# Performance work log

Hardware: AMD Instinct MI355X
Metric: run time of the kernel (lower is better)

Reference implementation:

```python
import jax, jax.numpy as jnp
from jax import lax
import numpy as np

T_STEPS, C_IN, H_IN, W_IN = 15, 6, 256, 256
C_OUT, KSIZE = 64, 5
THRESH = 15.0   # conv_t[0]
KWTA = 5        # ks[0]
INH_R = 3       # inh_radiuses[0]


def setup_inputs() -> dict:
    key = jax.random.key(0)
    k1, k2 = jax.random.split(key)
    # cumulative binary spike-wave: once a unit spikes it stays on (SpykeTorch convention)
    bern = jax.random.uniform(k1, (T_STEPS, C_IN, H_IN, W_IN)) < 0.05
    spikes = (jnp.cumsum(bern.astype(jnp.int32), axis=0) > 0).astype(jnp.float32)
    # SpykeTorch Convolution init: N(0.8, 0.05)
    w1 = 0.8 + 0.05 * jax.random.normal(k2, (C_OUT, C_IN, KSIZE, KSIZE), dtype=jnp.float32)
    return {"input": spikes, "w1": w1, "current_layer_id": 1}


def pointwise_inhibition(thr_pot):
    # thr_pot: (T, C, H, W). Keep, at each spatial position, only the feature
    # with the earliest spike (ties broken by max potential); zero the rest.
    T = thr_pot.shape[0]
    C = thr_pot.shape[1]
    max_vals = jnp.max(thr_pot, axis=1, keepdims=True)            # (T,1,H,W)
    max_idx = jnp.argmax(thr_pot, axis=1, keepdims=True)          # (T,1,H,W)
    clamp_pot = jnp.sign(max_vals)                                # (T,1,H,W) in {0,1}
    earliest = jnp.clip((T - clamp_pot.sum(axis=0, keepdims=True)).astype(jnp.int32), 0, T - 1)  # (1,1,H,W)
    winners = jnp.take_along_axis(max_idx, earliest, axis=0)      # (1,1,H,W)
    onehot = (jnp.arange(C)[None, :, None, None] == winners[:, 0])  # (1,C,H,W)
    coef = onehot.astype(thr_pot.dtype) * clamp_pot[-1:]          # zero where no spike at last step
    return thr_pot * coef


def get_k_winners(pot, spk, kwta, inh_radius):
    # pot, spk: (T, C, H, W). Returns (kwta, 3) int winners (c, h, w); -1 rows = no winner.
    T, C, H, W = pot.shape
    earliest = jnp.clip((T - spk.sum(axis=0, keepdims=True)).astype(jnp.int32), 0, T - 1)
    values = jnp.take_along_axis(pot, earliest, axis=0)           # (1,C,H,W)
    trunc = spk * values
    v = trunc.max() * T
    trunc = trunc + spk * v
    total = trunc.sum(axis=0)                                     # (C,H,W)
    rows = jnp.arange(H)
    cols = jnp.arange(W)

    def step(total, _):
        idx = jnp.argmax(total)
        val = total.reshape(-1)[idx]
        c = idx // (H * W)
        rem = idx % (H * W)
        h = rem // W
        w = rem % W
        winner = jnp.where(val != 0,
                           jnp.stack([c, h, w]),
                           jnp.full((3,), -1, dtype=idx.dtype))
        total = total.at[c].set(0.0)
        box = (((rows >= h - inh_radius) & (rows <= h + inh_radius))[:, None]
               & ((cols >= w - inh_radius) & (cols <= w + inh_radius))[None, :])
        total = jnp.where(box[None, :, :], 0.0, total)            # columnar spatial inhibition
        return total, winner

    _, winners = lax.scan(step, total, None, length=kwta)
    return winners


def reference(input, w1, current_layer_id):
    # training path, current_layer_id == 1
    x = jnp.pad(input.astype(jnp.float32), ((0, 0), (0, 0), (2, 2), (2, 2)))  # sf.pad (2,2,2,2)
    pot = lax.conv_general_dilated(x, w1, (1, 1), 'VALID',
                                   dimension_numbers=('NCHW', 'OIHW', 'NCHW'))  # (T,64,256,256)
    pot = jnp.where(pot < THRESH, 0.0, pot)   # sf.fire -> thresholded potentials
    pot = pointwise_inhibition(pot)
    spk = jnp.sign(pot)
    winners = get_k_winners(pot, spk, KWTA, INH_R)
    return spk, pot, winners
```

## Files before the change

### kernel.cpp

```cpp
#include <hip/hip_runtime.h>
#include <stdint.h>

static constexpr int T_STEPS = 15;
static constexpr int C_IN = 6;
static constexpr int C_OUT = 64;
static constexpr int H = 256;
static constexpr int W = 256;
static constexpr int NPOS = H * W;
static constexpr int NTAP = 150;
#define DTHRESH 15.0

typedef float vfloat4 __attribute__((ext_vector_type(4)));

static constexpr size_t WS_FT     = 0;
static constexpr size_t WS_SERIES = 393216;
static constexpr size_t WS_WINC   = WS_SERIES + (size_t)NPOS*16*4;
static constexpr size_t WS_NMAP   = WS_WINC + (size_t)NPOS;
static constexpr size_t WS_VAL    = WS_NMAP + (size_t)NPOS;
static constexpr size_t WS_NEED   = WS_VAL + (size_t)NPOS*8;

__global__ __launch_bounds__(256) void ft_kernel(const float* __restrict__ x,
                                                 uint8_t* __restrict__ ft) {
    int i = blockIdx.x * 256 + threadIdx.x;
    if (i >= C_IN * NPOS) return;
    int f = 15;
    #pragma unroll
    for (int t = T_STEPS - 1; t >= 0; --t) {
        if (x[(size_t)t * (C_IN * NPOS) + i] > 0.0f) f = t;
    }
    ft[i] = (uint8_t)f;
}

__global__ __launch_bounds__(256, 4) void conv_kernel(
        const float* __restrict__ w1, const uint8_t* __restrict__ ftg,
        float* __restrict__ series_ws, int8_t* __restrict__ winc_ws,
        uint8_t* __restrict__ nmap_ws, double* __restrict__ val_ws)
{
    __shared__ float w_lds[NTAP * 64];
    __shared__ uint8_t ft_lds[6 * 5 * 20];
    __shared__ alignas(16) unsigned cnt_lds[4][16];
    __shared__ alignas(16) unsigned short sorted_lds[4][200];

    int tid = threadIdx.x;
    int bid = blockIdx.x;
    int h  = bid >> 4;
    int w0 = (bid & 15) << 4;

    for (int i = tid; i < C_OUT * NTAP; i += 256) {
        int o = i / NTAP;
        int tap = i - o * NTAP;
        w_lds[tap * 64 + o] = w1[i];
    }
    for (int i = tid; i < 600; i += 256) {
        int c = i / 100;
        int r = i - c * 100;
        int kh = r / 20;
        int j  = r - kh * 20;
        int gh = h - 2 + kh;
        int gw = w0 - 2 + j;
        uint8_t v = 15;
        if (gh >= 0 && gh < H && gw >= 0 && gw < W) v = ftg[c * NPOS + gh * W + gw];
        ft_lds[(c * 5 + kh) * 20 + j] = v;
    }
    __syncthreads();

    int lane = tid & 63;
    int wvi  = tid >> 6;
    unsigned* cnt = cnt_lds[wvi];
    unsigned short* srt = sorted_lds[wvi];

    for (int iter = 0; iter < 4; ++iter) {
        int xl = iter * 4 + wvi;
        int p  = h * W + w0 + xl;

        if (lane < 16) cnt[lane] = 0;

        int tap0 = lane, tap1 = lane + 64, tap2 = lane + 128;
        auto ftv = [&](int tap) -> unsigned {
            int c = tap / 25;
            int r = tap - c * 25;
            int kh = r / 5;
            int kw = r - kh * 5;
            return ft_lds[(c * 5 + kh) * 20 + xl + kw];
        };
        unsigned f0 = ftv(tap0);
        unsigned f1 = ftv(tap1);
        unsigned f2 = (tap2 < NTAP) ? ftv(tap2) : 15u;
        unsigned r0 = 0, r1 = 0, r2 = 0;
        if (f0 < 15u) r0 = atomicAdd(&cnt[f0], 1u);
        if (f1 < 15u) r1 = atomicAdd(&cnt[f1], 1u);
        if (f2 < 15u) r2 = atomicAdd(&cnt[f2], 1u);

        uint4 c4[4];
        #pragma unroll
        for (int i = 0; i < 4; ++i) c4[i] = ((const uint4*)cnt)[i];
        unsigned cv_t[16];
        #pragma unroll
        for (int i = 0; i < 4; ++i) {
            cv_t[4*i+0] = c4[i].x; cv_t[4*i+1] = c4[i].y;
            cv_t[4*i+2] = c4[i].z; cv_t[4*i+3] = c4[i].w;
        }
        int kt[15];
        #pragma unroll
        for (int t = 0; t < 15; ++t) kt[t] = (int)__builtin_amdgcn_readfirstlane(cv_t[t]);

        unsigned st0 = 0, st1 = 0, st2 = 0;
        #pragma unroll
        for (int t = 0; t < 15; ++t) {
            unsigned a = (cv_t[t] + 3u) & ~3u;
            if ((unsigned)t < f0) st0 += a;
            if ((unsigned)t < f1) st1 += a;
            if ((unsigned)t < f2) st2 += a;
        }
        if (f0 < 15u) srt[st0 + r0] = (unsigned short)(tap0 << 6);
        if (f1 < 15u) srt[st1 + r1] = (unsigned short)(tap1 << 6);
        if (f2 < 15u) srt[st2 + r2] = (unsigned short)(tap2 << 6);

        double run = 0.0, cvv = 0.0;
        int tc = 127;
        float ser[15];
        int A = 0;
        #pragma unroll
        for (int t = 0; t < 15; ++t) {
            int k = kt[t];
            for (int q = 0; q < k; q += 4) {
                uint2 pr = *(const uint2*)(srt + A + q);
                unsigned e0 = pr.x & 0xFFFFu, e1 = pr.x >> 16;
                unsigned e2 = pr.y & 0xFFFFu, e3 = pr.y >> 16;
                e0 = min(e0, 9536u); e1 = min(e1, 9536u);
                e2 = min(e2, 9536u); e3 = min(e3, 9536u);
                float wa = w_lds[e0 + lane];
                float wb = w_lds[e1 + lane];
                float wcf = w_lds[e2 + lane];
                float wd = w_lds[e3 + lane];
                double p0 = (double)wa;
                double p1 = (q + 1 < k) ? (double)wb : 0.0;
                double p2 = (q + 2 < k) ? (double)wcf : 0.0;
                double p3 = (q + 3 < k) ? (double)wd : 0.0;
                run += ((p0 + p1) + (p2 + p3));
            }
            A += (k + 3) & ~3;
            ser[t] = (float)run;
            bool cross_now = (tc == 127) && (run >= DTHRESH);
            if (cross_now) { tc = t; cvv = run; }
        }

        int e = tc;
        #pragma unroll
        for (int off = 32; off >= 1; off >>= 1) e = min(e, __shfl_xor(e, off));
        int wc = -1;
        double val = 0.0;
        if (e < 15) {
            double vl = (tc == e) ? cvv : 0.0;
            double m = vl;
            #pragma unroll
            for (int off = 32; off >= 1; off >>= 1) m = fmax(m, __shfl_xor(m, off));
            unsigned long long mk = __ballot(vl == m);
            wc = __ffsll(mk) - 1;
            val = m;

            float ov = 0.0f;
            #pragma unroll
            for (int t = 0; t < 15; ++t) {
                float sv = __shfl(ser[t], wc);
                if (lane == t) ov = sv;
            }
            if (lane < e) ov = 0.0f;
            if (lane < 15) series_ws[p * 16 + lane] = ov;
        }
        if (lane == 0) {
            winc_ws[p] = (int8_t)wc;
            nmap_ws[p] = (uint8_t)(wc >= 0 ? (15 - e) : 0);
            if (wc >= 0) val_ws[p] = val;
        }
    }
}

__global__ __launch_bounds__(1024) void kwin_kernel(
        const int8_t* __restrict__ winc, const uint8_t* __restrict__ nmap,
        const double* __restrict__ val, float* __restrict__ outw)
{
    __shared__ int8_t  winc_l[NPOS];
    __shared__ uint8_t nmap_l[NPOS];
    __shared__ double rv_lds[16];
    __shared__ unsigned ri_lds[16];
    __shared__ double v_lds;
    __shared__ int win_c[5], win_h[5], win_w[5];
    int tid = threadIdx.x, lane = tid & 63, wvi = tid >> 6;

    {
        const int4* ws4 = (const int4*)winc;
        int4* wd4 = (int4*)winc_l;
        const int4* ns4 = (const int4*)nmap;
        int4* nd4 = (int4*)nmap_l;
        #pragma unroll
        for (int i = 0; i < NPOS / 16 / 1024; ++i) {
            wd4[tid + (i << 10)] = ws4[tid + (i << 10)];
            nd4[tid + (i << 10)] = ns4[tid + (i << 10)];
        }
    }
    __syncthreads();

    double mv = 0.0;
    for (int k = 0; k < 64; ++k) {
        int p = (k << 10) + tid;
        if (winc_l[p] >= 0) mv = fmax(mv, val[p]);
    }
    #pragma unroll
    for (int off = 32; off >= 1; off >>= 1) mv = fmax(mv, __shfl_xor(mv, off));
    if (lane == 0) rv_lds[wvi] = mv;
    __syncthreads();
    if (tid == 0) {
        double m = rv_lds[0];
        for (int i = 1; i < 16; ++i) m = fmax(m, rv_lds[i]);
        v_lds = 15.0 * m;
    }
    __syncthreads();
    double v = v_lds;

    for (int r = 0; r < 5; ++r) {
        int pc[5], ph[5], pw[5];
        #pragma unroll
        for (int j = 0; j < 5; ++j) { pc[j] = (j < r) ? win_c[j] : -99;
                                      ph[j] = (j < r) ? win_h[j] : -99;
                                      pw[j] = (j < r) ? win_w[j] : -99; }
        double bv = -1.0;
        unsigned bi = 0xFFFFFFFFu;
        for (int k = 0; k < 64; ++k) {
            int p = (k << 10) + tid;
            int c = winc_l[p];
            bool alive = (c >= 0);
            int hh = p >> 8, ww = p & 255;
            #pragma unroll
            for (int j = 0; j < 5; ++j) {
                bool kill = (c == pc[j]) ||
                            (hh >= ph[j] - 3 && hh <= ph[j] + 3 &&
                             ww >= pw[j] - 3 && ww <= pw[j] + 3);
                alive = alive && !kill;
            }
            if (alive) {
                double tot = (double)nmap_l[p] * (val[p] + v);
                unsigned fi = ((unsigned)c << 16) | (unsigned)p;
                if (tot > bv || (tot == bv && fi < bi)) { bv = tot; bi = fi; }
            }
        }
        #pragma unroll
        for (int off = 32; off >= 1; off >>= 1) {
            double ov = __shfl_xor(bv, off);
            unsigned oi = __shfl_xor(bi, off);
            if (ov > bv || (ov == bv && oi < bi)) { bv = ov; bi = oi; }
        }
        if (lane == 0) { rv_lds[wvi] = bv; ri_lds[wvi] = bi; }
        __syncthreads();
        if (tid == 0) {
            double bbv = rv_lds[0]; unsigned bbi = ri_lds[0];
            for (int i = 1; i < 16; ++i) {
                double ov = rv_lds[i]; unsigned oi = ri_lds[i];
                if (ov > bbv || (ov == bbv && oi < bbi)) { bbv = ov; bbi = oi; }
            }
            bool valid = (bbv > 0.0);
            int c = (int)(bbi >> 16), pp = (int)(bbi & 0xFFFFu);
            int hh = pp >> 8, ww = pp & 255;
            outw[r * 3 + 0] = valid ? (float)c  : -1.0f;
            outw[r * 3 + 1] = valid ? (float)hh : -1.0f;
            outw[r * 3 + 2] = valid ? (float)ww : -1.0f;
            win_c[r] = c; win_h[r] = hh; win_w[r] = ww;
        }
        __syncthreads();
    }
}

__global__ __launch_bounds__(256) void expand_kernel(
        const int8_t* __restrict__ winc, const float* __restrict__ series,
        float* __restrict__ spk, float* __restrict__ pot)
{
    int idx4 = blockIdx.x * 256 + threadIdx.x;
    int w4 = idx4 & 63;
    int h  = (idx4 >> 6) & 255;
    int c  = (idx4 >> 14) & 63;
    int t  = idx4 >> 20;
    int pbase = h * W + (w4 << 2);
    uint32_t wcs = *reinterpret_cast<const uint32_t*>(winc + pbase);
    vfloat4 pv = (vfloat4)(0.0f);
    vfloat4 sv = (vfloat4)(0.0f);
    #pragma unroll
    for (int e2 = 0; e2 < 4; ++e2) {
        int8_t wcb = (int8_t)((wcs >> (8 * e2)) & 0xFFu);
        if ((int)wcb == c) {
            float xv = series[(size_t)(pbase + e2) * 16 + t];
            pv[e2] = xv;
            sv[e2] = (xv > 0.f) ? 1.0f : 0.0f;
        }
    }
    reinterpret_cast<vfloat4*>(spk)[idx4] = sv;
    reinterpret_cast<vfloat4*>(pot)[idx4] = pv;
}

extern "C" void kernel_launch(void* const* d_in, const int* in_sizes, int n_in,
                              void* d_out, int out_size, void* d_ws, size_t ws_size,
                              hipStream_t stream)
{
    if (ws_size < WS_NEED) return;

    const float* x  = (const float*)d_in[0];
    const float* w1 = (const float*)d_in[1];
    uint8_t* ws = (uint8_t*)d_ws;
    uint8_t* ftg    = ws + WS_FT;
    float*   series = (float*)(ws + WS_SERIES);
    int8_t*  winc   = (int8_t*)(ws + WS_WINC);
    uint8_t* nmap   = (uint8_t*)(ws + WS_NMAP);
    double*  val    = (double*)(ws + WS_VAL);

    float* spk  = (float*)d_out;
    float* pot  = spk + (size_t)T_STEPS * C_OUT * NPOS;
    float* outw = pot + (size_t)T_STEPS * C_OUT * NPOS;

    hipLaunchKernelGGL(ft_kernel,     dim3(1536),  dim3(256),  0, stream, x, ftg);
    hipLaunchKernelGGL(conv_kernel,   dim3(4096),  dim3(256),  0, stream, w1, ftg, series, winc, nmap, val);
    hipLaunchKernelGGL(kwin_kernel,   dim3(1),     dim3(1024), 0, stream, winc, nmap, val, outw);
    hipLaunchKernelGGL(expand_kernel, dim3(61440), dim3(256),  0, stream, winc, series, spk, pot);
}
```

Baseline: 865.6 us.

## Parallelize k-winner selection across 256 blocks with cooperative grid sync

Replaces the single-block k-WTA kernel, which staged 128KB in LDS and scanned all positions serially per round, with a cooperative launch of 256 blocks where each thread owns one position. Global max and per-round argmax use wave shuffles, per-block partials in workspace, and grid.sync, with double-buffered reduction slots. Each thread keeps its alive flag in a register and updates it locally from the broadcast winner. This trades serial single-CU work for six grid-wide barriers and a cooperative launch.

New measurement: 867.8 us. About the same (+0.3%).

```diff
diff --git a/kernel.cpp b/kernel.cpp
--- a/kernel.cpp
+++ b/kernel.cpp
@@ -1,5 +1,8 @@
 #include <hip/hip_runtime.h>
+#include <hip/hip_cooperative_groups.h>
 #include <stdint.h>
+
+namespace cg = cooperative_groups;
 
 static constexpr int T_STEPS = 15;
 static constexpr int C_IN = 6;
@@ -17,7 +20,9 @@
 static constexpr size_t WS_WINC   = WS_SERIES + (size_t)NPOS*16*4;
 static constexpr size_t WS_NMAP   = WS_WINC + (size_t)NPOS;
 static constexpr size_t WS_VAL    = WS_NMAP + (size_t)NPOS;
-static constexpr size_t WS_NEED   = WS_VAL + (size_t)NPOS*8;
+static constexpr size_t WS_RED    = WS_VAL + (size_t)NPOS*8;
+static constexpr size_t WS_RIX    = WS_RED + 768*8;
+static constexpr size_t WS_NEED   = WS_RIX + 512*4;
 
 __global__ __launch_bounds__(256) void ft_kernel(const float* __restrict__ x,
                                                  uint8_t* __restrict__ ft) {
@@ -176,97 +181,100 @@
     }
 }
 
-__global__ __launch_bounds__(1024) void kwin_kernel(
+__global__ __launch_bounds__(256) void kwin_kernel(
         const int8_t* __restrict__ winc, const uint8_t* __restrict__ nmap,
-        const double* __restrict__ val, float* __restrict__ outw)
+        const double* __restrict__ val, float* __restrict__ outw,
+        double* __restrict__ redv, unsigned* __restrict__ redi)
 {
-    __shared__ int8_t  winc_l[NPOS];
-    __shared__ uint8_t nmap_l[NPOS];
-    __shared__ double rv_lds[16];
-    __shared__ unsigned ri_lds[16];
-    __shared__ double v_lds;
-    __shared__ int win_c[5], win_h[5], win_w[5];
-    int tid = threadIdx.x, lane = tid & 63, wvi = tid >> 6;
-
-    {
-        const int4* ws4 = (const int4*)winc;
-        int4* wd4 = (int4*)winc_l;
-        const int4* ns4 = (const int4*)nmap;
-        int4* nd4 = (int4*)nmap_l;
-        #pragma unroll
-        for (int i = 0; i < NPOS / 16 / 1024; ++i) {
-            wd4[tid + (i << 10)] = ws4[tid + (i << 10)];
-            nd4[tid + (i << 10)] = ns4[tid + (i << 10)];
-        }
-    }
-    __syncthreads();
-
-    double mv = 0.0;
-    for (int k = 0; k < 64; ++k) {
-        int p = (k << 10) + tid;
-        if (winc_l[p] >= 0) mv = fmax(mv, val[p]);
-    }
+    cg::grid_group grid = cg::this_grid();
+    const int tid  = threadIdx.x;
+    const int bid  = blockIdx.x;
+    const int p    = (bid << 8) | tid;
+    const int lane = tid & 63, wvi = tid >> 6;
+
+    __shared__ double   s_v[4];
+    __shared__ unsigned s_i[4];
+
+    const int    c     = winc[p];
+    const bool   owner = (c >= 0);
+    const double vp    = owner ? val[p] : 0.0;
+    const double nm    = (double)nmap[p];
+    const int    hh    = p >> 8;
+    const int    ww    = p & 255;
+    bool alive = owner;
+
+    double mv = vp;
     #pragma unroll
     for (int off = 32; off >= 1; off >>= 1) mv = fmax(mv, __shfl_xor(mv, off));
-    if (lane == 0) rv_lds[wvi] = mv;
+    if (lane == 0) s_v[wvi] = mv;
     __syncthreads();
-    if (tid == 0) {
-        double m = rv_lds[0];
-        for (int i = 1; i < 16; ++i) m = fmax(m, rv_lds[i]);
-        v_lds = 15.0 * m;
-    }
+    if (tid == 0)
+        redv[512 + bid] = fmax(fmax(s_v[0], s_v[1]), fmax(s_v[2], s_v[3]));
+    grid.sync();
+    double pv = redv[512 + tid];
+    #pragma unroll
+    for (int off = 32; off >= 1; off >>= 1) pv = fmax(pv, __shfl_xor(pv, off));
+    if (lane == 0) s_v[wvi] = pv;
     __syncthreads();
-    double v = v_lds;
+    const double v = 15.0 * fmax(fmax(s_v[0], s_v[1]), fmax(s_v[2], s_v[3]));
 
     for (int r = 0; r < 5; ++r) {
-        int pc[5], ph[5], pw[5];
-        #pragma unroll
-        for (int j = 0; j < 5; ++j) { pc[j] = (j < r) ? win_c[j] : -99;
-                                      ph[j] = (j < r) ? win_h[j] : -99;
-                                      pw[j] = (j < r) ? win_w[j] : -99; }
-        double bv = -1.0;
+        __syncthreads();
+        const int par = r & 1;
+
+        double   bv = -1.0;
         unsigned bi = 0xFFFFFFFFu;
-        for (int k = 0; k < 64; ++k) {
-            int p = (k << 10) + tid;
-            int c = winc_l[p];
-            bool alive = (c >= 0);
-            int hh = p >> 8, ww = p & 255;
-            #pragma unroll
-            for (int j = 0; j < 5; ++j) {
-                bool kill = (c == pc[j]) ||
-                            (hh >= ph[j] - 3 && hh <= ph[j] + 3 &&
-                             ww >= pw[j] - 3 && ww <= pw[j] + 3);
-                alive = alive && !kill;
-            }
-            if (alive) {
-                double tot = (double)nmap_l[p] * (val[p] + v);
-                unsigned fi = ((unsigned)c << 16) | (unsigned)p;
-                if (tot > bv || (tot == bv && fi < bi)) { bv = tot; bi = fi; }
-            }
+        if (alive) {
+            bv = nm * (vp + v);
+            bi = ((unsigned)c << 16) | (unsigned)p;
         }
         #pragma unroll
         for (int off = 32; off >= 1; off >>= 1) {
-            double ov = __shfl_xor(bv, off);
+            double   ov = __shfl_xor(bv, off);
             unsigned oi = __shfl_xor(bi, off);
             if (ov > bv || (ov == bv && oi < bi)) { bv = ov; bi = oi; }
         }
-        if (lane == 0) { rv_lds[wvi] = bv; ri_lds[wvi] = bi; }
+        if (lane == 0) { s_v[wvi] = bv; s_i[wvi] = bi; }
         __syncthreads();
         if (tid == 0) {
-            double bbv = rv_lds[0]; unsigned bbi = ri_lds[0];
-            for (int i = 1; i < 16; ++i) {
-                double ov = rv_lds[i]; unsigned oi = ri_lds[i];
-                if (ov > bbv || (ov == bbv && oi < bbi)) { bbv = ov; bbi = oi; }
-            }
-            bool valid = (bbv > 0.0);
-            int c = (int)(bbi >> 16), pp = (int)(bbi & 0xFFFFu);
-            int hh = pp >> 8, ww = pp & 255;
-            outw[r * 3 + 0] = valid ? (float)c  : -1.0f;
-            outw[r * 3 + 1] = valid ? (float)hh : -1.0f;
-            outw[r * 3 + 2] = valid ? (float)ww : -1.0f;
-            win_c[r] = c; win_h[r] = hh; win_w[r] = ww;
-        }
+            double bbv = s_v[0]; unsigned bbi = s_i[0];
+            #pragma unroll
+            for (int i = 1; i < 4; ++i)
+                if (s_v[i] > bbv || (s_v[i] == bbv && s_i[i] < bbi)) { bbv = s_v[i]; bbi = s_i[i]; }
+            redv[par * 256 + bid] = bbv;
+            redi[par * 256 + bid] = bbi;
+        }
+        grid.sync();
+
+        double   gv = redv[par * 256 + tid];
+        unsigned gi = redi[par * 256 + tid];
+        #pragma unroll
+        for (int off = 32; off >= 1; off >>= 1) {
+            double   ov = __shfl_xor(gv, off);
+            unsigned oi = __shfl_xor(gi, off);
+            if (ov > gv || (ov == gv && oi < gi)) { gv = ov; gi = oi; }
+        }
+        if (lane == 0) { s_v[wvi] = gv; s_i[wvi] = gi; }
         __syncthreads();
+        double bbv = s_v[0]; unsigned bbi = s_i[0];
+        #pragma unroll
+        for (int i = 1; i < 4; ++i)
+            if (s_v[i] > bbv || (s_v[i] == bbv && s_i[i] < bbi)) { bbv = s_v[i]; bbi = s_i[i]; }
+
+        const bool valid = (bbv > 0.0);
+        if (bid == 0 && tid == 0) {
+            int wc2 = (int)(bbi >> 16), pp = (int)(bbi & 0xFFFFu);
+            outw[r * 3 + 0] = valid ? (float)wc2       : -1.0f;
+            outw[r * 3 + 1] = valid ? (float)(pp >> 8) : -1.0f;
+            outw[r * 3 + 2] = valid ? (float)(pp & 255): -1.0f;
+        }
+        if (valid) {
+            const int wc2 = (int)(bbi >> 16);
+            const int wp  = (int)(bbi & 0xFFFFu);
+            const int wh  = wp >> 8, wwv = wp & 255;
+            if (c == wc2 || (hh >= wh - 3 && hh <= wh + 3 &&
+                             ww >= wwv - 3 && ww <= wwv + 3)) alive = false;
+        }
     }
 }
 
@@ -310,6 +318,8 @@
     int8_t*  winc   = (int8_t*)(ws + WS_WINC);
     uint8_t* nmap   = (uint8_t*)(ws + WS_NMAP);
     double*  val    = (double*)(ws + WS_VAL);
+    double*  redv   = (double*)(ws + WS_RED);
+    unsigned* redi  = (unsigned*)(ws + WS_RIX);
 
     float* spk  = (float*)d_out;
     float* pot  = spk + (size_t)T_STEPS * C_OUT * NPOS;
@@ -317,6 +327,10 @@
 
     hipLaunchKernelGGL(ft_kernel,     dim3(1536),  dim3(256),  0, stream, x, ftg);
     hipLaunchKernelGGL(conv_kernel,   dim3(4096),  dim3(256),  0, stream, w1, ftg, series, winc, nmap, val);
-    hipLaunchKernelGGL(kwin_kernel,   dim3(1),     dim3(1024), 0, stream, winc, nmap, val, outw);
+
+    void* kargs[] = { (void*)&winc, (void*)&nmap, (void*)&val,
+                      (void*)&outw, (void*)&redv, (void*)&redi };
+    hipLaunchCooperativeKernel((const void*)kwin_kernel, dim3(256), dim3(256), kargs, 0, stream);
+
     hipLaunchKernelGGL(expand_kernel, dim3(61440), dim3(256),  0, stream, winc, series, spk, pot);
 }
```
